# Optimization experiments

Hardware: AMD Instinct MI355X
Metric: run time of the kernel (lower is better)

Reference implementation:

```python
import jax, jax.numpy as jnp
import numpy as np

B, G, N_IN, N_HID, N_OUT = 2, 4096, 8, 32, 32
ALPHA, BETA, BN_EPS = 0.005, 5e-5, 1e-5
EDGE_P = 0.05  # adjacency density


def _lin_init(k, fan_in, fan_out):
    k1, k2 = jax.random.split(k)
    lim = 1.0 / np.sqrt(fan_in)
    W = jax.random.uniform(k1, (fan_in, fan_out), minval=-lim, maxval=lim, dtype=jnp.float32)
    b = jax.random.uniform(k2, (fan_out,), minval=-lim, maxval=lim, dtype=jnp.float32)
    return W, b


def setup_inputs() -> dict:
    key = jax.random.key(0)
    ks = jax.random.split(key, 12)
    W_infer, b_infer = _lin_init(ks[0], N_IN, N_HID)
    W_e1, b_e1 = _lin_init(ks[1], 2 * N_HID, 1)
    W_e2, b_e2 = _lin_init(ks[2], 2 * N_HID, 1)
    W_n1, b_n1 = _lin_init(ks[3], 2 * N_HID, N_OUT)
    W_n2, b_n2 = _lin_init(ks[4], 2 * N_HID, N_OUT)
    W_m1, b_m1 = _lin_init(ks[5], 2 * N_HID, N_OUT)
    W_m2, b_m2 = _lin_init(ks[6], 2 * N_HID, N_OUT)
    x = jax.random.normal(ks[7], (B, G, N_IN), dtype=jnp.float32)
    edges1 = jax.random.bernoulli(ks[8], EDGE_P, (G, G)).astype(jnp.float32)
    edges2 = jax.random.bernoulli(ks[9], EDGE_P, (G, G)).astype(jnp.float32)
    bn_gamma = jnp.ones((G,), jnp.float32)
    bn_beta = jnp.zeros((G,), jnp.float32)
    return dict(x=x, edges1=edges1, edges2=edges2, W_infer=W_infer, b_infer=b_infer,
                W_e1=W_e1, b_e1=b_e1, W_e2=W_e2, b_e2=b_e2,
                W_n1=W_n1, b_n1=b_n1, W_n2=W_n2, b_n2=b_n2,
                W_m1=W_m1, b_m1=b_m1, W_m2=W_m2, b_m2=b_m2,
                bn_gamma=bn_gamma, bn_beta=bn_beta)


def _mp_block(x, adj, coef, W_e, b_e, W_n, b_n, W_m, b_m):
    # x: [B,G,H]. Torch builds edge feature at flat index k=i*G+j as cat([x_j, x_i])
    # (shape2 = col gather, shape1 = row gather). We keep the same math without
    # materializing the [B,G*G,2H] tensor.
    Hh = x.shape[-1]
    s_src = x @ W_e[:Hh]   # [B,G,1]  (x_j part of mlp_edge)
    s_dst = x @ W_e[Hh:]   # [B,G,1]  (x_i part of mlp_edge)
    logits = s_dst[:, :, None, 0] + s_src[:, None, :, 0] + b_e[0]   # [B,G,G] at (i,j)
    w = adj + coef * (adj == 0).astype(x.dtype)                     # ori_edge + coef*thres_edge
    e = jax.nn.sigmoid(logits) * w[None]                            # [B,G,G]
    # receive at node i: sum_j e_ij * [x_j, x_i]
    recv_src = jnp.einsum('bij,bjh->bih', e, x)                     # sum_j e_ij x_j
    recv_dst = x * jnp.sum(e, axis=2)[..., None]                    # x_i * sum_j e_ij
    recv = jnp.concatenate([recv_src, recv_dst], axis=-1)           # [B,G,2H]
    recv = jax.nn.elu(recv @ W_n + b_n)                             # nodes_mlp + elu
    upd = jnp.concatenate([recv, x], axis=-1) @ W_m + b_m           # mesg_merge (mode='cat')
    return jax.nn.elu(upd)


def _forward(x, edges1, edges2, W_infer, b_infer, W_e1, b_e1, W_e2, b_e2,
             W_n1, b_n1, W_n2, b_n2, W_m1, b_m1, W_m2, b_m2, bn_gamma, bn_beta):
    h = jax.nn.elu(x @ W_infer + b_infer)                           # infer + elu, [B,G,H]
    h = _mp_block(h, edges1, ALPHA, W_e1, b_e1, W_n1, b_n1, W_m1, b_m1)
    # BatchNorm1d(gene_num) on [B, G, n_out]: per-gene stats over (batch, feature)
    mu = jnp.mean(h, axis=(0, 2), keepdims=True)
    var = jnp.var(h, axis=(0, 2), keepdims=True)
    h = (h - mu) * jax.lax.rsqrt(var + BN_EPS)
    h = h * bn_gamma[None, :, None] + bn_beta[None, :, None]
    return _mp_block(h, edges2, BETA, W_e2, b_e2, W_n2, b_n2, W_m2, b_m2)


def reference(x, edges1, edges2, W_infer, b_infer, W_e1, b_e1, W_e2, b_e2,
              W_n1, b_n1, W_n2, b_n2, W_m1, b_m1, W_m2, b_m2, bn_gamma, bn_beta):
    return _forward(x, edges1, edges2, W_infer, b_infer, W_e1, b_e1, W_e2, b_e2,
                    W_n1, b_n1, W_n2, b_n2, W_m1, b_m1, W_m2, b_m2, bn_gamma, bn_beta)
```

## Files before the change

### kernel.cpp

```cpp
#include <hip/hip_runtime.h>

#define G 4096
#define BSZ 2
#define NIN 8
#define HID 32
#define NLOG2E (-1.4426950408889634f)

typedef __attribute__((ext_vector_type(8))) short short8;
typedef __attribute__((ext_vector_type(4))) float floatx4;
typedef unsigned short ushort_t;
typedef unsigned int uint_t;

__device__ __forceinline__ float elu1(float v) {
    return v > 0.f ? v : (__expf(v) - 1.f);
}
__device__ __forceinline__ ushort_t f2bf(float f) {
    unsigned u = __float_as_uint(f);
    u += 0x7fffu + ((u >> 16) & 1u);
    return (ushort_t)(u >> 16);
}

__global__ __launch_bounds__(256) void k_setup1(
    const float* __restrict__ x, const float* __restrict__ W,
    const float* __restrict__ bias, const float* __restrict__ We,
    float* __restrict__ h0, ushort_t* __restrict__ hTb,
    float* __restrict__ ssrc, float* __restrict__ sdst) {
    __shared__ __align__(16) ushort_t hs[HID][264];
    int tid = threadIdx.x;
    int t = blockIdx.x * 256 + tid;
    int b = t >> 12;
    int g0 = (blockIdx.x & 15) * 256;
    float xin[NIN];
    const float* xp = x + t * NIN;
#pragma unroll
    for (int k = 0; k < NIN; k++) xin[k] = xp[k];
    float ss = 0.f, sd = 0.f;
    float* hp = h0 + (size_t)t * HID;
#pragma unroll
    for (int o = 0; o < HID; o++) {
        float v = bias[o];
#pragma unroll
        for (int k = 0; k < NIN; k++) v += xin[k] * W[k * HID + o];
        v = elu1(v);
        hp[o] = v;
        hs[o][tid] = f2bf(v);
        ss += v * We[o];
        sd += v * We[HID + o];
    }
    ssrc[t] = ss * NLOG2E;
    sdst[t] = sd * NLOG2E;
    __syncthreads();
#pragma unroll
    for (int p = 0; p < 4; p++) {
        int row = p * 8 + (tid >> 5);
        int c = (tid & 31) * 8;
        short8 v8 = *(const short8*)&hs[row][c];
        *(short8*)(void*)&hTb[(size_t)(b * HID + row) * G + g0 + c] = v8;
    }
}

template <bool DO_BN>
__global__ __launch_bounds__(512, 4) void k_fused(
    const float* __restrict__ adj, const float* __restrict__ ssrc,
    const float* __restrict__ sdst, const ushort_t* __restrict__ hTb_in,
    const float* __restrict__ bep, float coef, const float* __restrict__ hin,
    const float* __restrict__ Wn, const float* __restrict__ bnb,
    const float* __restrict__ Wm, const float* __restrict__ bmb,
    const float* __restrict__ gamma, const float* __restrict__ beta,
    const float* __restrict__ We2, float* __restrict__ outp,
    ushort_t* __restrict__ hTb_out, float* __restrict__ s2s,
    float* __restrict__ s2d) {
    union SMemU {
        float ssm[BSZ][G];
        struct {
            float rec[32][68];
            float rec2[32][68];
            float esg[16][2];
            ushort_t tb[BSZ][HID][16];
        } p;
    };
    __shared__ __align__(16) SMemU sm;
    __shared__ __align__(16) uint_t abits[128][17];
    __shared__ __align__(16) float red[6][64][9];
    __shared__ __align__(16) float Wns[2048];
    __shared__ __align__(16) float Wms[2048];

    int tid = threadIdx.x;
    int g0 = blockIdx.x * 16;
    int l = tid & 63, w = tid >> 6;
    int b = w >> 2, jq = w & 3;

    ((float4*)Wns)[tid] = ((const float4*)Wn)[tid];
    ((float4*)Wms)[tid] = ((const float4*)Wm)[tid];
#pragma unroll
    for (int r = 0; r < 4; r++) {
        int idx = r * 2048 + tid * 4;
        int bb = idx >> 12, j = idx & 4095;
        *(float4*)&sm.ssm[bb][j] = *(const float4*)&ssrc[bb * G + j];
    }

    int m = l & 15, kg = l >> 4;
    int jstart = jq * 1024;
    const ushort_t* hb0 = hTb_in + (size_t)(b * HID + m) * G + jstart + kg * 8;
    const ushort_t* hb1 = hb0 + (size_t)16 * G;
    short8 pb0[2], pb1[2];
#pragma unroll
    for (int d = 0; d < 2; d++) {
        pb0[d] = *(const short8*)(const void*)(hb0 + d * 32);
        pb1[d] = *(const short8*)(const void*)(hb1 + d * 32);
    }

    {
        const int sh2 = (tid & 7) * 4;
        const bool st = (tid & 7) == 0;
        const int wbase = tid >> 3;
        float4 ld[4];
#pragma unroll
        for (int bt = 0; bt < 8; bt++) {
            int r0 = bt * 2;
#pragma unroll
            for (int q = 0; q < 4; q++) {
                int r = r0 + (q >> 1), h = q & 1;
                ld[q] = *(const float4*)&adj[(size_t)(g0 + r) * G + (h * 512 + tid) * 4];
            }
#pragma unroll
            for (int q = 0; q < 4; q++) {
                int r = r0 + (q >> 1), h = q & 1;
                float4 v4 = ld[q];
                uint_t nib = (uint_t)(v4.x != 0.f) | ((uint_t)(v4.y != 0.f) << 1) |
                             ((uint_t)(v4.z != 0.f) << 2) | ((uint_t)(v4.w != 0.f) << 3);
                uint_t wd = nib << sh2;
                wd |= __shfl_xor(wd, 1);
                wd |= __shfl_xor(wd, 2);
                wd |= __shfl_xor(wd, 4);
                if (st) abits[h * 64 + wbase][r] = wd;
            }
        }
    }

    float sd2 = sdst[b * G + g0 + m] + bep[0] * NLOG2E;
    const float wm1 = 1.f - coef;
    floatx4 c0 = {0.f, 0.f, 0.f, 0.f}, c1 = {0.f, 0.f, 0.f, 0.f};
    float es = 0.f;
    __syncthreads();

    const float* svp = &sm.ssm[b][jstart + kg * 8];
    float4 sv0[2], sv1[2];
    uint_t bwr[2];
#pragma unroll
    for (int d = 0; d < 2; d++) {
        sv0[d] = *(const float4*)&svp[d * 32];
        sv1[d] = *(const float4*)&svp[d * 32 + 4];
        bwr[d] = abits[jq * 32 + d][m];
    }

#pragma unroll 4
    for (int jc = 0; jc < 32; jc++) {
        int lc = jc & 1;
        short8 bf0 = pb0[lc], bf1 = pb1[lc];
        float4 s0 = sv0[lc], s1 = sv1[lc];
        uint_t bw = bwr[lc];
        if (jc + 2 < 32) {
            pb0[lc] = *(const short8*)(const void*)(hb0 + (jc + 2) * 32);
            pb1[lc] = *(const short8*)(const void*)(hb1 + (jc + 2) * 32);
            sv0[lc] = *(const float4*)&svp[(jc + 2) * 32];
            sv1[lc] = *(const float4*)&svp[(jc + 2) * 32 + 4];
            bwr[lc] = abits[jq * 32 + jc + 2][m];
        }
        float sv[8] = {s0.x, s0.y, s0.z, s0.w, s1.x, s1.y, s1.z, s1.w};
        short8 af;
#pragma unroll
        for (int t8 = 0; t8 < 8; t8++) {
            float bitf = (float)((bw >> (kg * 8 + t8)) & 1u);
            float wgt = __builtin_fmaf(bitf, wm1, coef);
            float ex = exp2f(sd2 + sv[t8]);
            float e = __builtin_amdgcn_rcpf(1.f + ex) * wgt;
            es += e;
            af[t8] = (short)(__float_as_uint(e) >> 16);
        }
        c0 = __builtin_amdgcn_mfma_f32_16x16x32_bf16(af, bf0, c0, 0, 0, 0);
        c1 = __builtin_amdgcn_mfma_f32_16x16x32_bf16(af, bf1, c1, 0, 0, 0);
    }

    if (jq) {
        int widx = b * 3 + jq - 1;
#pragma unroll
        for (int r = 0; r < 4; r++) {
            red[widx][l][r] = c0[r];
            red[widx][l][4 + r] = c1[r];
        }
        red[widx][l][8] = es;
    }
    __syncthreads();
    if (!jq) {
#pragma unroll
        for (int q = 0; q < 3; q++) {
            int widx = b * 3 + q;
#pragma unroll
            for (int r = 0; r < 4; r++) {
                c0[r] += red[widx][l][r];
                c1[r] += red[widx][l][4 + r];
            }
            es += red[widx][l][8];
        }
        es += __shfl_xor(es, 16);
        es += __shfl_xor(es, 32);
#pragma unroll
        for (int r = 0; r < 4; r++) {
            int gene = (l >> 4) * 4 + r;
            sm.p.rec[gene * 2 + b][m] = c0[r];
            sm.p.rec[gene * 2 + b][16 + m] = c1[r];
        }
        if (l < 16) sm.p.esg[l][b] = es;
    }
    __syncthreads();

    int rl = tid >> 5, hh = tid & 31;
    float xv[2];
#pragma unroll
    for (int p = 0; p < 2; p++) {
        int rr = rl + p * 16, gene = rr >> 1, bb = rr & 1;
        xv[p] = hin[((size_t)(bb * G + g0 + gene)) * HID + hh];
        sm.p.rec[rr][32 + hh] = xv[p] * sm.p.esg[gene][bb];
    }
    __syncthreads();

#pragma unroll
    for (int p = 0; p < 2; p++) {
        int rr = rl + p * 16, gene = rr >> 1, bb = rr & 1;
        float v = bnb[hh];
#pragma unroll
        for (int k4 = 0; k4 < 16; k4++) {
            float4 r4 = *(const float4*)&sm.p.rec[rr][k4 * 4];
            v += r4.x * Wns[(k4 * 4 + 0) * HID + hh];
            v += r4.y * Wns[(k4 * 4 + 1) * HID + hh];
            v += r4.z * Wns[(k4 * 4 + 2) * HID + hh];
            v += r4.w * Wns[(k4 * 4 + 3) * HID + hh];
        }
        v = elu1(v);
        sm.p.rec2[rr][hh] = v;
        sm.p.rec2[rr][32 + hh] = xv[p];
        float u = bmb[hh];
#pragma unroll
        for (int k4 = 0; k4 < 16; k4++) {
            float4 r4 = *(const float4*)&sm.p.rec2[rr][k4 * 4];
            u += r4.x * Wms[(k4 * 4 + 0) * HID + hh];
            u += r4.y * Wms[(k4 * 4 + 1) * HID + hh];
            u += r4.z * Wms[(k4 * 4 + 2) * HID + hh];
            u += r4.w * Wms[(k4 * 4 + 3) * HID + hh];
        }
        float h1v = elu1(u);
        if (!DO_BN) {
            outp[((size_t)(bb * G + g0 + gene)) * HID + hh] = h1v;
        } else {
            float s = h1v, sq = h1v * h1v;
#pragma unroll
            for (int mm = 32; mm; mm >>= 1) {
                s += __shfl_xor(s, mm);
                sq += __shfl_xor(sq, mm);
            }
            float mu = s * (1.f / 64.f);
            float var = sq * (1.f / 64.f) - mu * mu;
            float rstd = rsqrtf(var + 1e-5f);
            float hn = (h1v - mu) * rstd * gamma[g0 + gene] + beta[g0 + gene];
            outp[((size_t)(bb * G + g0 + gene)) * HID + hh] = hn;
            sm.p.tb[bb][hh][gene] = f2bf(hn);
            float ps = hn * We2[hh], pd = hn * We2[HID + hh];
#pragma unroll
            for (int mm = 16; mm; mm >>= 1) {
                ps += __shfl_xor(ps, mm);
                pd += __shfl_xor(pd, mm);
            }
            if (hh == 0) {
                s2s[bb * G + g0 + gene] = ps * NLOG2E;
                s2d[bb * G + g0 + gene] = pd * NLOG2E;
            }
        }
    }
    if (DO_BN) {
        __syncthreads();
        if (tid < 128) {
            int b2 = tid >> 6, c = (tid >> 1) & 31, half = tid & 1;
            short8 v8 = *(const short8*)&sm.p.tb[b2][c][half * 8];
            *(short8*)(void*)&hTb_out[(size_t)(b2 * HID + c) * G + g0 + half * 8] = v8;
        }
    }
}

extern "C" void kernel_launch(void* const* d_in, const int* in_sizes, int n_in,
                              void* d_out, int out_size, void* d_ws, size_t ws_size,
                              hipStream_t stream) {
    const float* x      = (const float*)d_in[0];
    const float* edges1 = (const float*)d_in[1];
    const float* edges2 = (const float*)d_in[2];
    const float* W_inf  = (const float*)d_in[3];
    const float* b_inf  = (const float*)d_in[4];
    const float* W_e1   = (const float*)d_in[5];
    const float* b_e1   = (const float*)d_in[6];
    const float* W_e2   = (const float*)d_in[7];
    const float* b_e2   = (const float*)d_in[8];
    const float* W_n1   = (const float*)d_in[9];
    const float* b_n1   = (const float*)d_in[10];
    const float* W_n2   = (const float*)d_in[11];
    const float* b_n2   = (const float*)d_in[12];
    const float* W_m1   = (const float*)d_in[13];
    const float* b_m1   = (const float*)d_in[14];
    const float* W_m2   = (const float*)d_in[15];
    const float* b_m2   = (const float*)d_in[16];
    const float* bn_g   = (const float*)d_in[17];
    const float* bn_b   = (const float*)d_in[18];
    float* out = (float*)d_out;

    float* ws = (float*)d_ws;
    float* h0   = ws;
    float* h1n  = ws + 262144;
    float* s1s  = ws + 524288;
    float* s1d  = ws + 532480;
    float* s2s  = ws + 540672;
    float* s2d  = ws + 548864;
    ushort_t* hTb  = (ushort_t*)(ws + 557056);
    ushort_t* hTb2 = (ushort_t*)(ws + 688128);

    const float ALPHA = 0.005f, BETA = 5e-5f;

    k_setup1<<<32, 256, 0, stream>>>(x, W_inf, b_inf, W_e1, h0, hTb, s1s, s1d);
    k_fused<true><<<G / 16, 512, 0, stream>>>(
        edges1, s1s, s1d, hTb, b_e1, ALPHA, h0, W_n1, b_n1, W_m1, b_m1,
        bn_g, bn_b, W_e2, h1n, hTb2, s2s, s2d);
    k_fused<false><<<G / 16, 512, 0, stream>>>(
        edges2, s2s, s2d, hTb2, b_e2, BETA, h1n, W_n2, b_n2, W_m2, b_m2,
        nullptr, nullptr, nullptr, out, nullptr, nullptr, nullptr);
}
```

Baseline: 253.7 us.

## Split fused message-passing kernel into column-split MP and separate post-MLP kernels

The fused per-gene-block kernel becomes two kernels. The first splits the j dimension four ways across blocks, launching 1024 blocks instead of 256, and writes partial aggregations to workspace. The second reduces the four partials and runs the node MLP, merge MLP and BatchNorm. The aim is more parallelism and less per-block shared memory for the adjacency-streaming phase on a 256-CU device. The cost is two extra kernel launches and a global round trip for the partial sums.

Measured after the change: 229.7 us. 9.5% less time.

```diff
diff --git a/kernel.cpp b/kernel.cpp
--- a/kernel.cpp
+++ b/kernel.cpp
@@ -59,48 +59,22 @@
     }
 }
 
-template <bool DO_BN>
-__global__ __launch_bounds__(512, 4) void k_fused(
+__global__ __launch_bounds__(512, 2) void k_mp(
     const float* __restrict__ adj, const float* __restrict__ ssrc,
     const float* __restrict__ sdst, const ushort_t* __restrict__ hTb_in,
-    const float* __restrict__ bep, float coef, const float* __restrict__ hin,
-    const float* __restrict__ Wn, const float* __restrict__ bnb,
-    const float* __restrict__ Wm, const float* __restrict__ bmb,
-    const float* __restrict__ gamma, const float* __restrict__ beta,
-    const float* __restrict__ We2, float* __restrict__ outp,
-    ushort_t* __restrict__ hTb_out, float* __restrict__ s2s,
-    float* __restrict__ s2d) {
-    union SMemU {
-        float ssm[BSZ][G];
-        struct {
-            float rec[32][68];
-            float rec2[32][68];
-            float esg[16][2];
-            ushort_t tb[BSZ][HID][16];
-        } p;
-    };
-    __shared__ __align__(16) SMemU sm;
-    __shared__ __align__(16) uint_t abits[128][17];
+    const float* __restrict__ bep, float coef, float* __restrict__ pr) {
+    __shared__ __align__(16) float ssm[BSZ][1024];
+    __shared__ __align__(16) uint_t abits[32][17];
     __shared__ __align__(16) float red[6][64][9];
-    __shared__ __align__(16) float Wns[2048];
-    __shared__ __align__(16) float Wms[2048];
 
     int tid = threadIdx.x;
-    int g0 = blockIdx.x * 16;
+    int gblk = blockIdx.x >> 2, jh = blockIdx.x & 3;
+    int g0 = gblk * 16, j0 = jh * 1024;
     int l = tid & 63, w = tid >> 6;
     int b = w >> 2, jq = w & 3;
-
-    ((float4*)Wns)[tid] = ((const float4*)Wn)[tid];
-    ((float4*)Wms)[tid] = ((const float4*)Wm)[tid];
-#pragma unroll
-    for (int r = 0; r < 4; r++) {
-        int idx = r * 2048 + tid * 4;
-        int bb = idx >> 12, j = idx & 4095;
-        *(float4*)&sm.ssm[bb][j] = *(const float4*)&ssrc[bb * G + j];
-    }
-
     int m = l & 15, kg = l >> 4;
-    int jstart = jq * 1024;
+
+    int jstart = j0 + jq * 256;
     const ushort_t* hb0 = hTb_in + (size_t)(b * HID + m) * G + jstart + kg * 8;
     const ushort_t* hb1 = hb0 + (size_t)16 * G;
     short8 pb0[2], pb1[2];
@@ -111,30 +85,24 @@
     }
 
     {
-        const int sh2 = (tid & 7) * 4;
-        const bool st = (tid & 7) == 0;
-        const int wbase = tid >> 3;
-        float4 ld[4];
-#pragma unroll
-        for (int bt = 0; bt < 8; bt++) {
-            int r0 = bt * 2;
-#pragma unroll
-            for (int q = 0; q < 4; q++) {
-                int r = r0 + (q >> 1), h = q & 1;
-                ld[q] = *(const float4*)&adj[(size_t)(g0 + r) * G + (h * 512 + tid) * 4];
-            }
-#pragma unroll
-            for (int q = 0; q < 4; q++) {
-                int r = r0 + (q >> 1), h = q & 1;
-                float4 v4 = ld[q];
-                uint_t nib = (uint_t)(v4.x != 0.f) | ((uint_t)(v4.y != 0.f) << 1) |
-                             ((uint_t)(v4.z != 0.f) << 2) | ((uint_t)(v4.w != 0.f) << 3);
-                uint_t wd = nib << sh2;
-                wd |= __shfl_xor(wd, 1);
-                wd |= __shfl_xor(wd, 2);
-                wd |= __shfl_xor(wd, 4);
-                if (st) abits[h * 64 + wbase][r] = wd;
-            }
+        int bb = tid >> 8, j4 = tid & 255;
+        *(float4*)&ssm[bb][j4 * 4] = *(const float4*)&ssrc[bb * G + j0 + j4 * 4];
+    }
+    {
+        int r = tid >> 8, f4 = tid & 255;
+        int word = f4 >> 3;
+        int sh2 = (tid & 7) * 4;
+        bool st = (tid & 7) == 0;
+#pragma unroll
+        for (int rr = 0; rr < 8; rr++) {
+            float4 v4 = *(const float4*)&adj[(size_t)(g0 + rr * 2 + r) * G + j0 + f4 * 4];
+            uint_t nib = (uint_t)(v4.x != 0.f) | ((uint_t)(v4.y != 0.f) << 1) |
+                         ((uint_t)(v4.z != 0.f) << 2) | ((uint_t)(v4.w != 0.f) << 3);
+            uint_t wd = nib << sh2;
+            wd |= __shfl_xor(wd, 1);
+            wd |= __shfl_xor(wd, 2);
+            wd |= __shfl_xor(wd, 4);
+            if (st) abits[word][rr * 2 + r] = wd;
         }
     }
 
@@ -144,28 +112,28 @@
     float es = 0.f;
     __syncthreads();
 
-    const float* svp = &sm.ssm[b][jstart + kg * 8];
+    const float* svp = &ssm[b][jq * 256 + kg * 8];
     float4 sv0[2], sv1[2];
     uint_t bwr[2];
 #pragma unroll
     for (int d = 0; d < 2; d++) {
         sv0[d] = *(const float4*)&svp[d * 32];
         sv1[d] = *(const float4*)&svp[d * 32 + 4];
-        bwr[d] = abits[jq * 32 + d][m];
-    }
-
-#pragma unroll 4
-    for (int jc = 0; jc < 32; jc++) {
+        bwr[d] = abits[jq * 8 + d][m];
+    }
+
+#pragma unroll
+    for (int jc = 0; jc < 8; jc++) {
         int lc = jc & 1;
         short8 bf0 = pb0[lc], bf1 = pb1[lc];
         float4 s0 = sv0[lc], s1 = sv1[lc];
         uint_t bw = bwr[lc];
-        if (jc + 2 < 32) {
+        if (jc + 2 < 8) {
             pb0[lc] = *(const short8*)(const void*)(hb0 + (jc + 2) * 32);
             pb1[lc] = *(const short8*)(const void*)(hb1 + (jc + 2) * 32);
             sv0[lc] = *(const float4*)&svp[(jc + 2) * 32];
             sv1[lc] = *(const float4*)&svp[(jc + 2) * 32 + 4];
-            bwr[lc] = abits[jq * 32 + jc + 2][m];
+            bwr[lc] = abits[jq * 8 + jc + 2][m];
         }
         float sv[8] = {s0.x, s0.y, s0.z, s0.w, s1.x, s1.y, s1.z, s1.w};
         short8 af;
@@ -205,83 +173,103 @@
         }
         es += __shfl_xor(es, 16);
         es += __shfl_xor(es, 32);
+        float* prb = pr + (size_t)blockIdx.x * 1056;
 #pragma unroll
         for (int r = 0; r < 4; r++) {
             int gene = (l >> 4) * 4 + r;
-            sm.p.rec[gene * 2 + b][m] = c0[r];
-            sm.p.rec[gene * 2 + b][16 + m] = c1[r];
-        }
-        if (l < 16) sm.p.esg[l][b] = es;
-    }
+            int row = gene * 2 + b;
+            prb[row * 32 + m] = c0[r];
+            prb[row * 32 + 16 + m] = c1[r];
+        }
+        if (l < 16) prb[1024 + l * 2 + b] = es;
+    }
+}
+
+template <bool DO_BN>
+__global__ __launch_bounds__(1024, 4) void k_post(
+    const float* __restrict__ pr, const float* __restrict__ hin,
+    const float* __restrict__ Wn, const float* __restrict__ bnb,
+    const float* __restrict__ Wm, const float* __restrict__ bmb,
+    const float* __restrict__ gamma, const float* __restrict__ beta,
+    const float* __restrict__ We2, float* __restrict__ outp,
+    ushort_t* __restrict__ hTb_out, float* __restrict__ s2s,
+    float* __restrict__ s2d) {
+    __shared__ __align__(16) float rec[32][68];
+    __shared__ __align__(16) float rec2[32][68];
+    __shared__ __align__(16) ushort_t tb[BSZ][HID][16];
+    __shared__ __align__(16) float Wns[2048];
+    __shared__ __align__(16) float Wms[2048];
+
+    int tid = threadIdx.x;
+    int g0 = blockIdx.x * 16;
+    if (tid < 512) {
+        ((float4*)Wns)[tid] = ((const float4*)Wn)[tid];
+    } else {
+        ((float4*)Wms)[tid - 512] = ((const float4*)Wm)[tid - 512];
+    }
+    int rl = tid >> 5, hh = tid & 31;
+    int gene = rl >> 1, bb = rl & 1;
+    const float* p0 = pr + (size_t)blockIdx.x * 4 * 1056;
+    float rv = p0[rl * 32 + hh] + p0[1056 + rl * 32 + hh] +
+               p0[2112 + rl * 32 + hh] + p0[3168 + rl * 32 + hh];
+    float esv = p0[1024 + rl] + p0[1056 + 1024 + rl] +
+                p0[2112 + 1024 + rl] + p0[3168 + 1024 + rl];
+    float xv = hin[((size_t)(bb * G + g0 + gene)) * HID + hh];
+    rec[rl][hh] = rv;
+    rec[rl][32 + hh] = xv * esv;
     __syncthreads();
 
-    int rl = tid >> 5, hh = tid & 31;
-    float xv[2];
-#pragma unroll
-    for (int p = 0; p < 2; p++) {
-        int rr = rl + p * 16, gene = rr >> 1, bb = rr & 1;
-        xv[p] = hin[((size_t)(bb * G + g0 + gene)) * HID + hh];
-        sm.p.rec[rr][32 + hh] = xv[p] * sm.p.esg[gene][bb];
-    }
-    __syncthreads();
-
-#pragma unroll
-    for (int p = 0; p < 2; p++) {
-        int rr = rl + p * 16, gene = rr >> 1, bb = rr & 1;
-        float v = bnb[hh];
-#pragma unroll
-        for (int k4 = 0; k4 < 16; k4++) {
-            float4 r4 = *(const float4*)&sm.p.rec[rr][k4 * 4];
-            v += r4.x * Wns[(k4 * 4 + 0) * HID + hh];
-            v += r4.y * Wns[(k4 * 4 + 1) * HID + hh];
-            v += r4.z * Wns[(k4 * 4 + 2) * HID + hh];
-            v += r4.w * Wns[(k4 * 4 + 3) * HID + hh];
-        }
-        v = elu1(v);
-        sm.p.rec2[rr][hh] = v;
-        sm.p.rec2[rr][32 + hh] = xv[p];
-        float u = bmb[hh];
-#pragma unroll
-        for (int k4 = 0; k4 < 16; k4++) {
-            float4 r4 = *(const float4*)&sm.p.rec2[rr][k4 * 4];
-            u += r4.x * Wms[(k4 * 4 + 0) * HID + hh];
-            u += r4.y * Wms[(k4 * 4 + 1) * HID + hh];
-            u += r4.z * Wms[(k4 * 4 + 2) * HID + hh];
-            u += r4.w * Wms[(k4 * 4 + 3) * HID + hh];
-        }
-        float h1v = elu1(u);
-        if (!DO_BN) {
-            outp[((size_t)(bb * G + g0 + gene)) * HID + hh] = h1v;
-        } else {
-            float s = h1v, sq = h1v * h1v;
-#pragma unroll
-            for (int mm = 32; mm; mm >>= 1) {
-                s += __shfl_xor(s, mm);
-                sq += __shfl_xor(sq, mm);
-            }
-            float mu = s * (1.f / 64.f);
-            float var = sq * (1.f / 64.f) - mu * mu;
-            float rstd = rsqrtf(var + 1e-5f);
-            float hn = (h1v - mu) * rstd * gamma[g0 + gene] + beta[g0 + gene];
-            outp[((size_t)(bb * G + g0 + gene)) * HID + hh] = hn;
-            sm.p.tb[bb][hh][gene] = f2bf(hn);
-            float ps = hn * We2[hh], pd = hn * We2[HID + hh];
-#pragma unroll
-            for (int mm = 16; mm; mm >>= 1) {
-                ps += __shfl_xor(ps, mm);
-                pd += __shfl_xor(pd, mm);
-            }
-            if (hh == 0) {
-                s2s[bb * G + g0 + gene] = ps * NLOG2E;
-                s2d[bb * G + g0 + gene] = pd * NLOG2E;
-            }
-        }
-    }
-    if (DO_BN) {
+    float v = bnb[hh];
+#pragma unroll
+    for (int k4 = 0; k4 < 16; k4++) {
+        float4 r4 = *(const float4*)&rec[rl][k4 * 4];
+        v += r4.x * Wns[(k4 * 4 + 0) * HID + hh];
+        v += r4.y * Wns[(k4 * 4 + 1) * HID + hh];
+        v += r4.z * Wns[(k4 * 4 + 2) * HID + hh];
+        v += r4.w * Wns[(k4 * 4 + 3) * HID + hh];
+    }
+    v = elu1(v);
+    rec2[rl][hh] = v;
+    rec2[rl][32 + hh] = xv;
+    float u = bmb[hh];
+#pragma unroll
+    for (int k4 = 0; k4 < 16; k4++) {
+        float4 r4 = *(const float4*)&rec2[rl][k4 * 4];
+        u += r4.x * Wms[(k4 * 4 + 0) * HID + hh];
+        u += r4.y * Wms[(k4 * 4 + 1) * HID + hh];
+        u += r4.z * Wms[(k4 * 4 + 2) * HID + hh];
+        u += r4.w * Wms[(k4 * 4 + 3) * HID + hh];
+    }
+    float h1v = elu1(u);
+    if (!DO_BN) {
+        outp[((size_t)(bb * G + g0 + gene)) * HID + hh] = h1v;
+    } else {
+        float s = h1v, sq = h1v * h1v;
+#pragma unroll
+        for (int mm = 32; mm; mm >>= 1) {
+            s += __shfl_xor(s, mm);
+            sq += __shfl_xor(sq, mm);
+        }
+        float mu = s * (1.f / 64.f);
+        float var = sq * (1.f / 64.f) - mu * mu;
+        float rstd = rsqrtf(var + 1e-5f);
+        float hn = (h1v - mu) * rstd * gamma[g0 + gene] + beta[g0 + gene];
+        outp[((size_t)(bb * G + g0 + gene)) * HID + hh] = hn;
+        tb[bb][hh][gene] = f2bf(hn);
+        float ps = hn * We2[hh], pd = hn * We2[HID + hh];
+#pragma unroll
+        for (int mm = 16; mm; mm >>= 1) {
+            ps += __shfl_xor(ps, mm);
+            pd += __shfl_xor(pd, mm);
+        }
+        if (hh == 0) {
+            s2s[bb * G + g0 + gene] = ps * NLOG2E;
+            s2d[bb * G + g0 + gene] = pd * NLOG2E;
+        }
         __syncthreads();
         if (tid < 128) {
             int b2 = tid >> 6, c = (tid >> 1) & 31, half = tid & 1;
-            short8 v8 = *(const short8*)&sm.p.tb[b2][c][half * 8];
+            short8 v8 = *(const short8*)&tb[b2][c][half * 8];
             *(short8*)(void*)&hTb_out[(size_t)(b2 * HID + c) * G + g0 + half * 8] = v8;
         }
     }
@@ -320,14 +308,17 @@
     float* s2d  = ws + 548864;
     ushort_t* hTb  = (ushort_t*)(ws + 557056);
     ushort_t* hTb2 = (ushort_t*)(ws + 688128);
+    float* pr = ws + 819200;
 
     const float ALPHA = 0.005f, BETA = 5e-5f;
 
     k_setup1<<<32, 256, 0, stream>>>(x, W_inf, b_inf, W_e1, h0, hTb, s1s, s1d);
-    k_fused<true><<<G / 16, 512, 0, stream>>>(
-        edges1, s1s, s1d, hTb, b_e1, ALPHA, h0, W_n1, b_n1, W_m1, b_m1,
-        bn_g, bn_b, W_e2, h1n, hTb2, s2s, s2d);
-    k_fused<false><<<G / 16, 512, 0, stream>>>(
-        edges2, s2s, s2d, hTb2, b_e2, BETA, h1n, W_n2, b_n2, W_m2, b_m2,
-        nullptr, nullptr, nullptr, out, nullptr, nullptr, nullptr);
-}
+    k_mp<<<1024, 512, 0, stream>>>(edges1, s1s, s1d, hTb, b_e1, ALPHA, pr);
+    k_post<true><<<256, 1024, 0, stream>>>(
+        pr, h0, W_n1, b_n1, W_m1, b_m1, bn_g, bn_b, W_e2,
+        h1n, hTb2, s2s, s2d);
+    k_mp<<<1024, 512, 0, stream>>>(edges2, s2s, s2d, hTb2, b_e2, BETA, pr);
+    k_post<false><<<256, 1024, 0, stream>>>(
+        pr, h1n, W_n2, b_n2, W_m2, b_m2, nullptr, nullptr, nullptr,
+        out, nullptr, nullptr, nullptr);
+}
```
